# Kernel tuning notes

Hardware: AMD Instinct MI355X
Metric: run time of the kernel (lower is better)

Reference implementation:

```python
import jax, jax.numpy as jnp
import numpy as np

T = 3              # num_ntype (slots)
NH = 64            # num_hidden == num_classes
HEADS = (4, 4, 1)
NUM_ETYPES = 5
EDGE_DIM = 64
N_NODES = 20000
NEG_SLOPE = 0.2
ALPHA = 0.05       # residual-attention blend
EPS = 1e-12


def _l2_by_slot(x):
    # l2_norm with l2BySlot='True': normalize each ntype slot independently
    n = x.shape[0]
    xs = x.reshape(n, T, -1)
    nrm = jnp.linalg.norm(xs, axis=2, keepdims=True)
    return (xs / jnp.maximum(nrm, EPS)).reshape(n, -1)


def _edge_softmax(logits, dst, n):
    # softmax over incoming edges of each destination node
    m = jax.lax.stop_gradient(jax.ops.segment_max(logits, dst, num_segments=n))
    e = jnp.exp(logits - m[dst])
    s = jax.ops.segment_sum(e, dst, num_segments=n)
    return e / s[dst]


def _conv(x, src, dst, etype, W, al, ar, ee_tab, We, ae, res_attn, act):
    # slotGATConv: x [N,T,C], W [T,C,H*O], al/ar [H,T*O], ee_tab [R,De], We [De,H*De], ae [H,De]
    n = x.shape[0]
    H = al.shape[0]
    proj = jnp.einsum('ntc,tcd->ntd', x, W)                     # [N,T,H*O]
    O = proj.shape[-1] // H
    feat = proj.reshape(n, T, H, O).transpose(0, 2, 1, 3).reshape(n, H, T * O)
    el = jnp.einsum('nhd,hd->nh', feat, al)
    er = jnp.einsum('nhd,hd->nh', feat, ar)
    De = ee_tab.shape[1]
    ep = (ee_tab[etype] @ We).reshape(-1, H, De)                # [E,H,De]
    ee = jnp.einsum('ehd,hd->eh', ep, ae)                       # [E,H]
    logit = jax.nn.leaky_relu(el[src] + er[dst] + ee, NEG_SLOPE)
    a = _edge_softmax(logit, dst, n)                            # [E,H]
    if res_attn is not None:
        a = a * (1.0 - ALPHA) + res_attn * ALPHA
    out = jax.ops.segment_sum(feat[src] * a[:, :, None], dst, num_segments=n)  # [N,H,T*O]
    if act:
        out = jax.nn.elu(out)
    return out, a


def _forward(feat0, feat1, feat2, w_in0, b_in0, w_in1, b_in1, w_in2, b_in2,
             l0_W, l0_al, l0_ar, l0_ee, l0_we, l0_ae,
             l1_W, l1_al, l1_ar, l1_ee, l1_we, l1_ae,
             l2_W, l2_al, l2_ar, l2_ee, l2_we, l2_ae,
             dm_W, e_feat, src, dst, left, right, mid):
    feats = [feat0, feat1, feat2]
    lins = [(w_in0, b_in0), (w_in1, b_in1), (w_in2, b_in2)]
    blocks = []
    for t, (f, (w, b)) in enumerate(zip(feats, lins)):
        ft = f @ w + b                                          # [n_t, NH]
        pad = jnp.zeros((f.shape[0], T * NH), ft.dtype)
        blocks.append(pad.at[:, t * NH:(t + 1) * NH].set(ft))   # slot zero-padding
    h = jnp.concatenate(blocks, 0)                              # [N, T*NH]
    emb = [_l2_by_slot(h)]                                      # aggregator='None' -> identity
    x = h.reshape(-1, T, NH)
    out0, a0 = _conv(x, src, dst, e_feat, l0_W, l0_al, l0_ar, l0_ee, l0_we, l0_ae, None, True)
    emb.append(_l2_by_slot(out0.mean(1)))
    x = out0.reshape(-1, HEADS[0], T, NH).transpose(0, 2, 1, 3).reshape(-1, T, HEADS[0] * NH)
    out1, a1 = _conv(x, src, dst, e_feat, l1_W, l1_al, l1_ar, l1_ee, l1_we, l1_ae, a0, True)
    emb.append(_l2_by_slot(out1.mean(1)))
    x = out1.reshape(-1, HEADS[1], T, NH).transpose(0, 2, 1, 3).reshape(-1, T, HEADS[1] * NH)
    out2, _ = _conv(x, src, dst, e_feat, l2_W, l2_al, l2_ar, l2_ee, l2_we, l2_ae, a1, False)
    emb.append(_l2_by_slot(out2.mean(1)))
    # aggregator='None' + inProcessEmb='True': concat per-slot along feature dim
    embs = [e.reshape(-1, T, NH) for e in emb]
    o = jnp.concatenate(embs, 2).reshape(-1, T * NH * len(embs))  # [N, 768]
    le, re = o[left], o[right]
    scores = jnp.zeros(left.shape[0], o.dtype)
    for r in range(NUM_ETYPES):                                 # DistMult per relation
        s = ((le @ dm_W[r]) * re).sum(1)
        scores = jnp.where(mid == r, s, scores)
    return jax.nn.sigmoid(scores)


def setup_inputs() -> dict:
    key = jax.random.key(0)
    ks = iter(jax.random.split(key, 64))
    def nrm(shape, std):
        return jax.random.normal(next(ks), shape, jnp.float32) * std
    counts = [8000, 6000, 6000]
    in_dims = [256, 128, 64]
    inp = {}
    for t in range(T):
        inp[f'feat{t}'] = jax.random.normal(next(ks), (counts[t], in_dims[t]), jnp.float32)
        inp[f'w_in{t}'] = nrm((in_dims[t], NH), 0.1)
        inp[f'b_in{t}'] = nrm((NH,), 0.1)
    Cs = [NH, HEADS[0] * NH, HEADS[1] * NH]
    for l in range(3):
        H = HEADS[l]
        inp[f'l{l}_W'] = nrm((T, Cs[l], H * NH), 0.1)
        inp[f'l{l}_al'] = nrm((H, T * NH), 0.1)
        inp[f'l{l}_ar'] = nrm((H, T * NH), 0.1)
        inp[f'l{l}_ee'] = nrm((NUM_ETYPES, EDGE_DIM), 0.1)
        inp[f'l{l}_we'] = nrm((EDGE_DIM, H * EDGE_DIM), 0.1)
        inp[f'l{l}_ae'] = nrm((H, EDGE_DIM), 0.1)
    D = T * NH * 4
    inp['dm_W'] = nrm((NUM_ETYPES, D, D), 0.05)
    E, L = 200000, 10000
    inp['e_feat'] = jax.random.randint(next(ks), (E,), 0, NUM_ETYPES)
    inp['src'] = jax.random.randint(next(ks), (E,), 0, N_NODES)
    inp['dst'] = jax.random.randint(next(ks), (E,), 0, N_NODES)
    inp['left'] = jax.random.randint(next(ks), (L,), 0, N_NODES)
    inp['right'] = jax.random.randint(next(ks), (L,), 0, N_NODES)
    inp['mid'] = jax.random.randint(next(ks), (L,), 0, NUM_ETYPES)
    return inp


def reference(feat0, feat1, feat2, w_in0, b_in0, w_in1, b_in1, w_in2, b_in2,
              l0_W, l0_al, l0_ar, l0_ee, l0_we, l0_ae,
              l1_W, l1_al, l1_ar, l1_ee, l1_we, l1_ae,
              l2_W, l2_al, l2_ar, l2_ee, l2_we, l2_ae,
              dm_W, e_feat, src, dst, left, right, mid):
    return _forward(feat0, feat1, feat2, w_in0, b_in0, w_in1, b_in1, w_in2, b_in2,
                    l0_W, l0_al, l0_ar, l0_ee, l0_we, l0_ae,
                    l1_W, l1_al, l1_ar, l1_ee, l1_we, l1_ae,
                    l2_W, l2_al, l2_ar, l2_ee, l2_we, l2_ae,
                    dm_W, e_feat, src, dst, left, right, mid)
```

## Files before the change

kernel.cpp:

```cpp
#include <hip/hip_runtime.h>
#include <math.h>

#define N_NODES 20000
#define NPAD    20096
#define N_EDGES 200000
#define N_PAIRS 10000
#define PAIR_PAD 10368
#define DM_TILES 162
#define NBLK    79

typedef __attribute__((ext_vector_type(8))) short s16x8;
typedef __attribute__((ext_vector_type(4))) float f32x4;

__device__ inline float wave_max(float v){
  for (int o = 32; o > 0; o >>= 1) v = fmaxf(v, __shfl_xor(v, o));
  return v;
}
__device__ inline float wave_sum(float v){
  for (int o = 32; o > 0; o >>= 1) v += __shfl_xor(v, o);
  return v;
}
__device__ inline short f2bf(float x){
  union { float f; unsigned u; } v; v.f = x;
  unsigned r = (v.u + 0x7FFFu + ((v.u >> 16) & 1u)) >> 16;
  return (short)r;
}
__device__ inline float bf2f(short s){
  union { unsigned u; float f; } v; v.u = ((unsigned)(unsigned short)s) << 16;
  return v.f;
}
__device__ inline int ntype(int s){ return (s < 8000) ? 0 : ((s < 14000) ? 1 : 2); }
__device__ inline float elu1(float x){ return (x > 0.f) ? x : expm1f(x); }

#define OS(i, c) ((i) * 100 + (c))

__global__ void build_h(const float* __restrict__ f0, const float* __restrict__ w0, const float* __restrict__ b0,
                        const float* __restrict__ f1, const float* __restrict__ w1, const float* __restrict__ b1,
                        const float* __restrict__ f2, const float* __restrict__ w2, const float* __restrict__ b2,
                        short* __restrict__ Xb0, short* __restrict__ o_b,
                        int* __restrict__ cnt3, int* __restrict__ cnt5, int* __restrict__ pos5,
                        float* __restrict__ score, int* __restrict__ pairs,
                        float* __restrict__ eall, short* __restrict__ Xb12,
                        short* __restrict__ featb){
  const int blk = blockIdx.x, lane = threadIdx.x;
  const int gid = blk * 64 + lane;
  if (gid < 80000) cnt3[gid] = 0;
  if (gid < 5){ cnt5[gid * 16] = 0; pos5[gid * 16] = 0; }
  if (gid < 10016) score[gid] = 0.f;
  if (gid < PAIR_PAD) pairs[gid] = -1;
  for (int i = gid; i < 480000; i += 160000) eall[i] = 0.f;
  s16x8 z = {};
  if (gid < 4608){
    int t = (gid * 16) / 24576, off = (gid * 16) % 24576;
    short* p = Xb12 + ((size_t)(t * NPAD + N_NODES)) * 256 + off;
    *(s16x8*)p = z; *(s16x8*)(p + 8) = z;
  }
  if (gid < 1152){
    int t = (gid * 16) / 6144, off = (gid * 16) % 6144;
    short* p = Xb0 + ((size_t)(t * NPAD + N_NODES)) * 64 + off;
    *(s16x8*)p = z; *(s16x8*)(p + 8) = z;
  }
  int t, C, nbase; const float *f, *w, *b;
  if (blk < 1000)       { t = 0; nbase = 0;     C = 256; f = f0; w = w0; b = b0; }
  else if (blk < 1750)  { t = 1; nbase = 8000;  C = 128; f = f1; w = w1; b = b1; }
  else                  { t = 2; nbase = 14000; C = 64;  f = f2; w = w2; b = b2; }
  const int n0 = blk * 8;
  const int n0l = n0 - nbase;
  __shared__ float xs[8 * 256];
  const float* fr = f + (size_t)n0l * C;
  for (int i = lane; i < 8 * C; i += 64) xs[i] = fr[i];
  __syncthreads();
  float acc[8];
#pragma unroll
  for (int j = 0; j < 8; j++) acc[j] = b[lane];
  for (int c = 0; c < C; c++){
    float wv = w[c * 64 + lane];
#pragma unroll
    for (int j = 0; j < 8; j++) acc[j] += xs[j * C + c] * wv;
  }
  for (int j = 0; j < 8; j++){
    int n = n0 + j;
    {
      int h = lane >> 4, si = (lane >> 3) & 1, j8 = lane & 7;
      int s0 = (t == 0) ? 1 : 0;
      int s1 = (t == 2) ? 1 : 2;
      int toff = si ? s1 : s0;
      *(s16x8*)(featb + ((size_t)n * 4 + h) * 192 + toff * 64 + j8 * 8) = z;
    }
    for (int tt = 0; tt < 3; tt++)
      Xb0[((size_t)(tt * NPAD) + n) * 64 + lane] = f2bf((tt == t) ? acc[j] : 0.f);
    float ss = wave_sum(acc[j] * acc[j]);
    float sc = 1.f / fmaxf(sqrtf(ss), 1e-12f);
    for (int tt = 0; tt < 3; tt++)
      o_b[(size_t)n * 768 + tt * 256 + lane] = f2bf((tt == t) ? acc[j] * sc : 0.f);
  }
}

__global__ void count_prep_k(const int* __restrict__ dst, const int* __restrict__ srcv,
                             int* __restrict__ cnt3,
                             const int* __restrict__ mid, int* __restrict__ cnt5,
                             const float* __restrict__ lW0, const float* __restrict__ lW1,
                             const float* __restrict__ lW2, const float* __restrict__ dmW,
// ... 181 lines not shown
  __shared__ __attribute__((aligned(16))) short A_s[128 * 32];
  __shared__ __attribute__((aligned(16))) short B_s[64 * 32];
  const short* Xt  = Xb + (size_t)t * NPAD * C;
  const short* Wtt = Wt + ((size_t)t * NO + ct * 64) * C;
  f32x4 acc[2][4] = {};
  for (int kk = 0; kk < C; kk += 32){
    {
      int row = tid >> 1, half = tid & 1;
      const s16x8* g = (const s16x8*)(Xt + (size_t)(n0 + row) * C + kk + half * 16);
      s16x8 v0 = g[0], v1 = g[1];
      *(s16x8*)(A_s + row * 32 + half * 16) = v0;
      *(s16x8*)(A_s + row * 32 + half * 16 + 8) = v1;
    }
    {
      int row = tid >> 2, chunk = tid & 3;
      s16x8 v = *(const s16x8*)(Wtt + (size_t)row * C + kk + chunk * 8);
      *(s16x8*)(B_s + row * 32 + chunk * 8) = v;
    }
    __syncthreads();
    s16x8 af0 = *(s16x8*)(A_s + (w * 32 + ln) * 32 + quad * 8);
    s16x8 af1 = *(s16x8*)(A_s + (w * 32 + 16 + ln) * 32 + quad * 8);
    s16x8 bf[4];
#pragma unroll
    for (int b = 0; b < 4; b++) bf[b] = *(s16x8*)(B_s + (b * 16 + ln) * 32 + quad * 8);
#pragma unroll
    for (int b = 0; b < 4; b++){
      acc[0][b] = __builtin_amdgcn_mfma_f32_16x16x32_bf16(af0, bf[b], acc[0][b], 0, 0, 0);
      acc[1][b] = __builtin_amdgcn_mfma_f32_16x16x32_bf16(af1, bf[b], acc[1][b], 0, 0, 0);
    }
    __syncthreads();
  }
#pragma unroll
  for (int ar_ = 0; ar_ < 2; ar_++){
#pragma unroll
    for (int i = 0; i < 4; i++){
      int n = n0 + w * 32 + ar_ * 16 + quad * 4 + i;
      if (n >= N_NODES) continue;
#pragma unroll
      for (int b = 0; b < 4; b++){
        int jj = b * 16 + ln;
        featb[((size_t)n * H + ct) * 192 + t * 64 + jj] = f2bf(acc[ar_][b][i]);
      }
    }
  }
  float alv[4], arv[4];
#pragma unroll
  for (int b = 0; b < 4; b++){
    alv[b] = al[ct * 192 + t * 64 + b * 16 + ln];
    arv[b] = ar[ct * 192 + t * 64 + b * 16 + ln];
  }
#pragma unroll
  for (int ar_ = 0; ar_ < 2; ar_++){
#pragma unroll
    for (int i = 0; i < 4; i++){
      float pe = 0.f, pr = 0.f;
#pragma unroll
      for (int b = 0; b < 4; b++){
        pe += acc[ar_][b][i] * alv[b];
        pr += acc[ar_][b][i] * arv[b];
      }
#pragma unroll
      for (int o = 1; o < 16; o <<= 1){
        pe += __shfl_xor(pe, o);
        pr += __shfl_xor(pr, o);
      }
      int n = n0 + w * 32 + ar_ * 16 + quad * 4 + i;
      if (ln == 0 && n < N_NODES){
        atomicAdd(&elf[n * H + ct], pe);
        atomicAdd(&erf[n * H + ct], pr);
      }
    }
  }
}

template<int H, int MODE, int ACT, int TYPED>
__global__ __launch_bounds__(256) void gat_fused(
    const int* __restrict__ csr_off, const int* __restrict__ src_sorted,
    const int* __restrict__ et_sorted,
    const float* __restrict__ el, const float* __restrict__ er, const float* __restrict__ ee5,
    const float* __restrict__ aprev, float* __restrict__ aout,
    const short* __restrict__ featb, short* __restrict__ outb,
    short* __restrict__ o_b, const int* __restrict__ cnt3, int kslice){
  const int wid = threadIdx.x >> 6, lane = threadIdx.x & 63;
  const int n = blockIdx.x * 4 + wid;
  if (n >= N_NODES) return;
  const int off = csr_off[n];
  const int cnt = csr_off[n + 1] - off;
  __shared__ float a_s[4][64][H];
  __shared__ int   src_s[4][64];
  __shared__ float out_s[4][800];
  float ern[H];
  if constexpr (H == 4){
    f32x4 ev = *(const f32x4*)(er + n * 4);
#pragma unroll
    for (int h = 0; h < 4; h++) ern[h] = ev[h];
  } else {
    ern[0] = er[n];
  }

  if (cnt <= 64){
    int p = off + lane;
    int sidx = 0, r = 0;
    if (lane < cnt){ sidx = src_sorted[p]; r = et_sorted[p]; }
    int src0 = __shfl(sidx, 0);
    src_s[wid][lane] = ((lane < cnt) ? sidx : src0) * (H * 384);
    float lg[H];
#pragma unroll
    for (int h = 0; h < H; h++) lg[h] = -1e30f;
    if (lane < cnt){
      if constexpr (H == 4){
        f32x4 elv = *(const f32x4*)(el + sidx * 4);
        f32x4 eev = *(const f32x4*)(ee5 + r * 4);
#pragma unroll
        for (int h = 0; h < 4; h++){
          float v = elv[h] + ern[h] + eev[h];
          lg[h] = (v >= 0.f) ? v : 0.2f * v;
        }
      } else {
        float v = el[sidx] + ern[0] + ee5[r];
        lg[0] = (v >= 0.f) ? v : 0.2f * v;
      }
    }
    float ap[4] = {};
    if (MODE > 0 && lane < cnt){
      f32x4 av4 = *(const f32x4*)(aprev + (size_t)p * 4);
#pragma unroll
      for (int q = 0; q < 4; q++) ap[q] = av4[q];
    }
    float av[H];
#pragma unroll
    for (int h = 0; h < H; h++){
      float mh = wave_max(lg[h]);
      float ex = (lane < cnt) ? __expf(lg[h] - mh) : 0.f;
      float sh = wave_sum(ex);
      float a = ex / sh;
      if (MODE == 1) a = 0.95f * a + 0.05f * ap[h];
      if (MODE == 2) a = 0.95f * a + 0.0125f * (ap[0] + ap[1] + ap[2] + ap[3]);
      av[h] = a;
      a_s[wid][lane][h] = (lane < cnt) ? a : 0.f;
    }
    if constexpr (MODE != 2){
      if (lane < cnt){
        f32x4 o = {av[0], av[1], av[2], av[3]};
        *(f32x4*)(aout + (size_t)p * 4) = o;
      }
    }
    const char* fb = (const char*)featb;

    if constexpr (TYPED && H == 4){
      const int q = lane & 31, eo = lane >> 5;
      const int hh = q >> 3, j8 = q & 7;
      float acc[3][8] = {};
      const int b1 = cnt3[n * 4], b2 = b1 + cnt3[n * 4 + 1];
      const int rb[4] = {0, b1, b2, cnt};
#pragma unroll
      for (int t = 0; t < 3; t++){
        const int sub = hh * 384 + t * 128 + j8 * 16;
        for (int b = rb[t]; b < rb[t + 1]; b += 2){
          int e = b + eo;
          bool vld = e < rb[t + 1];
          int ei = vld ? e : rb[t + 1] - 1;
          int so = src_s[wid][ei];
          float a = vld ? a_s[wid][ei][hh] : 0.f;
          s16x8 fv = *(const s16x8*)(fb + so + sub);
#pragma unroll
          for (int i = 0; i < 8; i++) acc[t][i] += a * bf2f(fv[i]);
        }
      }
#pragma unroll
      for (int t = 0; t < 3; t++){
#pragma unroll
        for (int i = 0; i < 8; i++){
          float tot = acc[t][i] + __shfl_xor(acc[t][i], 32);
          if (ACT) tot = elu1(tot);
          if (lane < 32) out_s[wid][OS(i, hh * 24 + t * 8 + j8)] = tot;
        }
      }
    } else if constexpr (H == 4){
      const int p0 = lane;
      const int p1 = (lane < 32) ? lane + 64 : lane - 32;
      const int p2 = lane + 32;
      const int hA = p0 / 24, hB = p1 / 24, hC = p2 / 24;
      const int eo2 = lane >> 5;
      float acc0[8] = {}, acc1[8] = {}, acc2[8] = {};
      const int cnt4 = (cnt + 3) & ~3;
      for (int b = 0; b < cnt4; b += 4){
        int eB0 = b + eo2, eB1 = b + 2 + eo2;
        int oA0 = src_s[wid][b],     oB0 = src_s[wid][eB0], oC0 = src_s[wid][b + 1];
        int oA1 = src_s[wid][b + 2], oB1 = src_s[wid][eB1], oC1 = src_s[wid][b + 3];
        float aA0 = a_s[wid][b][hA],     aB0 = a_s[wid][eB0][hB], aC0 = a_s[wid][b + 1][hC];
        float aA1 = a_s[wid][b + 2][hA], aB1 = a_s[wid][eB1][hB], aC1 = a_s[wid][b + 3][hC];
        s16x8 fA0 = *(const s16x8*)(fb + oA0 + p0 * 16);
        s16x8 fB0 = *(const s16x8*)(fb + oB0 + p1 * 16);
        s16x8 fC0 = *(const s16x8*)(fb + oC0 + p2 * 16);
        s16x8 fA1 = *(const s16x8*)(fb + oA1 + p0 * 16);
        s16x8 fB1 = *(const s16x8*)(fb + oB1 + p1 * 16);
        s16x8 fC1 = *(const s16x8*)(fb + oC1 + p2 * 16);
#pragma unroll
        for (int i = 0; i < 8; i++){
          acc0[i] += aA0 * bf2f(fA0[i]) + aA1 * bf2f(fA1[i]);
          acc1[i] += aB0 * bf2f(fB0[i]) + aB1 * bf2f(fB1[i]);
          acc2[i] += aC0 * bf2f(fC0[i]) + aC1 * bf2f(fC1[i]);
        }
      }
#pragma unroll
      for (int i = 0; i < 8; i++){
        float v1 = (lane < 32) ? acc2[i] : acc1[i];
        float r1 = __shfl_xor(v1, 32);
        float v0 = acc0[i] + r1;
        if (ACT) v0 = elu1(v0);
        out_s[wid][OS(i, p0)] = v0;
        float r2 = __shfl_xor(acc2[i], 32);
        if (lane < 32){
          float vv = acc1[i] + r2;
          if (ACT) vv = elu1(vv);
          out_s[wid][OS(i, p1)] = vv;
        }
      }
    } else {
      const int eo = lane & 7, cb = lane >> 3;
      float acc[3][8] = {};
      for (int b = 0; b < cnt; b += 8){
        int e = b + eo;
        float a = a_s[wid][e][0];
        int so = src_s[wid][e];
#pragma unroll
        for (int c = 0; c < 3; c++){
          s16x8 fv = *(const s16x8*)(fb + so + (cb * 3 + c) * 16);
#pragma unroll
          for (int i = 0; i < 8; i++) acc[c][i] += a * bf2f(fv[i]);
        }
      }
#pragma unroll
      for (int c = 0; c < 3; c++){
#pragma unroll
        for (int i = 0; i < 8; i++){
          float v = acc[c][i];
          v += __shfl_xor(v, 1); v += __shfl_xor(v, 2); v += __shfl_xor(v, 4);
          if (ACT) v = elu1(v);
          if (eo == 0) out_s[wid][OS(i, cb * 3 + c)] = v;
        }
      }
    }
  } else {
    constexpr int NC = H * 192 / 8;
    const int c0 = lane, h0 = (c0 / 24) % H;
    const int c1 = lane + 64, h1 = (c1 / 24) % H;
    const bool act0 = (c0 < NC);
    const bool act1 = (H == 4) && (lane < 32);
    float acc0[8] = {}, acc1[8] = {};
    float mh[H], sh[H];
#pragma unroll
    for (int h = 0; h < H; h++){ mh[h] = -1e30f; sh[h] = 0.f; }
    for (int b = lane; b < cnt; b += 64){
      int p = off + b; int s = src_sorted[p]; int r = et_sorted[p];
#pragma unroll
      for (int h = 0; h < H; h++){
        float v = el[s * H + h] + ern[h] + ee5[r * H + h];
        v = (v >= 0.f) ? v : 0.2f * v;
        mh[h] = fmaxf(mh[h], v);
      }
    }
#pragma unroll
    for (int h = 0; h < H; h++) mh[h] = wave_max(mh[h]);
    for (int b = lane; b < cnt; b += 64){
      int p = off + b; int s = src_sorted[p]; int r = et_sorted[p];
#pragma unroll
      for (int h = 0; h < H; h++){
        float v = el[s * H + h] + ern[h] + ee5[r * H + h];
        v = (v >= 0.f) ? v : 0.2f * v;
        sh[h] += __expf(v - mh[h]);
      }
    }
#pragma unroll
    for (int h = 0; h < H; h++) sh[h] = wave_sum(sh[h]);
    if (MODE != 2){
      for (int b = lane; b < cnt; b += 64){
        int p = off + b; int s = src_sorted[p]; int r = et_sorted[p];
        float ap[4] = {};
        if (MODE > 0){
#pragma unroll
          for (int q = 0; q < 4; q++) ap[q] = aprev[(size_t)p * 4 + q];
        }
        float av[4] = {};
#pragma unroll
        for (int h = 0; h < H; h++){
          float v = el[s * H + h] + ern[h] + ee5[r * H + h];
          v = (v >= 0.f) ? v : 0.2f * v;
          float a = __expf(v - mh[h]) / sh[h];
          if (MODE == 1) a = 0.95f * a + 0.05f * ap[h];
          av[h] = a;
        }
        f32x4 o = {av[0], av[1], av[2], av[3]};
        *(f32x4*)(aout + (size_t)p * 4) = o;
      }
    }
    for (int b = 0; b < cnt; b++){
      int p = off + b; int s = src_sorted[p]; int r = et_sorted[p];
      const short* row = featb + (size_t)s * (H * 192);
      float apm[4] = {};
      if (MODE > 0){
#pragma unroll
        for (int q = 0; q < 4; q++) apm[q] = aprev[(size_t)p * 4 + q];
      }
      if (act0){
        float v = el[s * H + h0] + ern[h0] + ee5[r * H + h0];
        v = (v >= 0.f) ? v : 0.2f * v;
        float a = __expf(v - mh[h0]) / sh[h0];
        if (MODE == 1) a = 0.95f * a + 0.05f * apm[h0];
        if (MODE == 2) a = 0.95f * a + 0.0125f * (apm[0] + apm[1] + apm[2] + apm[3]);
        s16x8 vv = *(const s16x8*)(row + c0 * 8);
#pragma unroll
        for (int i = 0; i < 8; i++) acc0[i] += a * bf2f(vv[i]);
      }
      if (act1){
        float v = el[s * H + h1] + ern[h1] + ee5[r * H + h1];
        v = (v >= 0.f) ? v : 0.2f * v;
        float a = __expf(v - mh[h1]) / sh[h1];
        if (MODE == 1) a = 0.95f * a + 0.05f * apm[h1];
        s16x8 vv = *(const s16x8*)(row + c1 * 8);
#pragma unroll
        for (int i = 0; i < 8; i++) acc1[i] += a * bf2f(vv[i]);
      }
    }
    if (act0){
#pragma unroll
      for (int i = 0; i < 8; i++){
        float v = ACT ? elu1(acc0[i]) : acc0[i];
        out_s[wid][OS(i, c0)] = v;
      }
    }
    if (act1){
#pragma unroll
      for (int i = 0; i < 8; i++){
        float v = ACT ? elu1(acc1[i]) : acc1[i];
        out_s[wid][OS(i, c1)] = v;
      }
    }
  }

  constexpr int NC = H * 192 / 8;
  if (outb){
    {
      const int c0 = lane;
      if (c0 < NC){
        int dd = c0 * 8, h = dd / 192, rr = dd % 192, t = rr / 64, j = rr % 64;
        s16x8 o;
#pragma unroll
        for (int i = 0; i < 8; i++) o[i] = f2bf(out_s[wid][OS(i, c0)]);
        *(s16x8*)(outb + ((size_t)(t * NPAD) + n) * 256 + h * 64 + j) = o;
      }
    }
    if constexpr (H == 4){
      if (lane < 32){
        const int c1 = lane + 64;
        int dd = c1 * 8, h = dd / 192, rr = dd % 192, t = rr / 64, j = rr % 64;
        s16x8 o;
#pragma unroll
        for (int i = 0; i < 8; i++) o[i] = f2bf(out_s[wid][OS(i, c1)]);
        *(s16x8*)(outb + ((size_t)(t * NPAD) + n) * 256 + h * 64 + j) = o;
      }
    }
  }
  for (int t = 0; t < 3; t++){
    float v;
    if (H == 4){
      int d0 = t * 64 + lane;
      v = 0.25f * (out_s[wid][OS(d0 & 7, d0 >> 3)] +
                   out_s[wid][OS(d0 & 7, 24 + (d0 >> 3))] +
                   out_s[wid][OS(d0 & 7, 48 + (d0 >> 3))] +
                   out_s[wid][OS(d0 & 7, 72 + (d0 >> 3))]);
    } else {
      int d0 = t * 64 + lane;
      v = out_s[wid][OS(d0 & 7, d0 >> 3)];
    }
    float ss = wave_sum(v * v);
    float sc = 1.f / fmaxf(sqrtf(ss), 1e-12f);
    o_b[(size_t)n * 768 + t * 256 + kslice * 64 + lane] = f2bf(v * sc);
  }
}

__global__ void distmult_mfma(const short* __restrict__ o_b, const short* __restrict__ Mt,
                              const int* __restrict__ pairs, const int* __restrict__ left,
                              const int* __restrict__ right, const int* __restrict__ mid,
                              float* __restrict__ score){
  const int pt = blockIdx.x, ct = blockIdx.y;
  const int tid = threadIdx.x;
  const int w = tid >> 6, lane = tid & 63;
  const int quad = lane >> 4, ln = lane & 15;
  __shared__ __attribute__((aligned(16))) short smem[8192];
  short* A_s = smem;
  short* B_s = smem + 2048;
  __shared__ int pid_s[64];
  __shared__ int lbase[64];
  if (tid < 64){
    int p = pairs[pt * 64 + tid];
    pid_s[tid] = p;
    lbase[tid] = (p >= 0) ? left[p] * 768 : 0;
  }
  __syncthreads();
  int p0 = pid_s[0];
  if (p0 < 0) return;
  const int r = mid[p0];
  const short* Mr = Mt + (size_t)r * 768 * 768;
  f32x4 acc[8] = {};
  for (int kk = 0; kk < 768; kk += 32){
    {
      int row = tid >> 2, chunk = tid & 3;
      s16x8 v = *(const s16x8*)(o_b + (size_t)lbase[row] + kk + chunk * 8);
      *(s16x8*)(A_s + row * 32 + chunk * 8) = v;
    }
    {
      int row = tid >> 1, half = tid & 1;
      const s16x8* g = (const s16x8*)(Mr + (size_t)(ct * 128 + row) * 768 + kk + half * 16);
      s16x8 v0 = g[0], v1 = g[1];
      *(s16x8*)(B_s + row * 32 + half * 16) = v0;
      *(s16x8*)(B_s + row * 32 + half * 16 + 8) = v1;
    }
    __syncthreads();
    s16x8 af = *(s16x8*)(A_s + (w * 16 + ln) * 32 + quad * 8);
#pragma unroll
    for (int b = 0; b < 8; b++){
      s16x8 bf = *(s16x8*)(B_s + (b * 16 + ln) * 32 + quad * 8);
      acc[b] = __builtin_amdgcn_mfma_f32_16x16x32_bf16(af, bf, acc[b], 0, 0, 0);
    }
    __syncthreads();
  }
  short* RE_s = smem;
  {
    int row = tid >> 2, quarter = tid & 3;
    int p = pid_s[row];
    s16x8 v0 = {}, v1 = {}, v2 = {}, v3 = {};
    if (p >= 0){
      const s16x8* g = (const s16x8*)(o_b + (size_t)right[p] * 768 + ct * 128 + quarter * 32);
      v0 = g[0]; v1 = g[1]; v2 = g[2]; v3 = g[3];
    }
    __syncthreads();
    short* dst = RE_s + row * 128 + quarter * 32;
    *(s16x8*)(dst)      = v0;
    *(s16x8*)(dst + 8)  = v1;
    *(s16x8*)(dst + 16) = v2;
    *(s16x8*)(dst + 24) = v3;
  }
  __syncthreads();
#pragma unroll
  for (int i = 0; i < 4; i++){
    int row = w * 16 + quad * 4 + i;
    float s = 0.f;
#pragma unroll
    for (int b = 0; b < 8; b++)
      s += acc[b][i] * bf2f(RE_s[row * 128 + b * 16 + ln]);
    s += __shfl_xor(s, 1); s += __shfl_xor(s, 2);
    s += __shfl_xor(s, 4); s += __shfl_xor(s, 8);
    if (ln == 0){
      int p = pid_s[row];
      if (p >= 0) atomicAdd(&score[p], s);
    }
  }
}

__global__ void sigmoid_k(const float* __restrict__ score, float* __restrict__ out){
  int i = blockIdx.x * 256 + threadIdx.x;
  if (i < N_PAIRS) out[i] = 1.f / (1.f + __expf(-score[i]));
}

extern "C" void kernel_launch(void* const* d_in, const int* in_sizes, int n_in,
                              void* d_out, int out_size, void* d_ws, size_t ws_size,
                              hipStream_t stream){
  const float* f0 = (const float*)d_in[0];
  const float* w0 = (const float*)d_in[1];
  const float* b0 = (const float*)d_in[2];
  const float* f1 = (const float*)d_in[3];
  const float* w1 = (const float*)d_in[4];
  const float* b1 = (const float*)d_in[5];
  const float* f2 = (const float*)d_in[6];
  const float* w2_ = (const float*)d_in[7];
  const float* b2 = (const float*)d_in[8];
  const float* lW[3]  = {(const float*)d_in[9],  (const float*)d_in[15], (const float*)d_in[21]};
  const float* lal[3] = {(const float*)d_in[10], (const float*)d_in[16], (const float*)d_in[22]};
  const float* lar[3] = {(const float*)d_in[11], (const float*)d_in[17], (const float*)d_in[23]};
  const float* lee[3] = {(const float*)d_in[12], (const float*)d_in[18], (const float*)d_in[24]};
  const float* lwe[3] = {(const float*)d_in[13], (const float*)d_in[19], (const float*)d_in[25]};
  const float* lae[3] = {(const float*)d_in[14], (const float*)d_in[20], (const float*)d_in[26]};
  const float* dmW = (const float*)d_in[27];
  const int* efeat = (const int*)d_in[28];
  const int* srcv  = (const int*)d_in[29];
  const int* dstv  = (const int*)d_in[30];
  const int* left  = (const int*)d_in[31];
  const int* right = (const int*)d_in[32];
  const int* midv  = (const int*)d_in[33];
  float* out = (float*)d_out;

  short* feat_b = (short*)d_ws;
  float* aA     = (float*)(feat_b + 15360000);
  float* aB     = aA + 800000;
  float* eall   = aB + 800000;
  float* ee5f   = eall + 480000;
  float* score  = ee5f + 96;
  int* cnt3     = (int*)(score + 10016);
  int* csr_off  = cnt3 + 80000;
  int* csr_pos  = csr_off + 20004;
  int* loc      = csr_pos + 80000;
  int* bsum     = loc + 20000;
  int* bofs     = bsum + 128;
  int* src_sorted = bofs + 128;
  int* et_sorted  = src_sorted + 200000;
  int* cnt5     = et_sorted + 200000;
  int* off5     = cnt5 + 80;
  int* pos5     = off5 + 8;
  int* pairs    = pos5 + 80;
  short* o_b    = (short*)(pairs + PAIR_PAD);
  short* Xb0    = o_b + 15360000;
  short* Xb12   = Xb0 + 3858432;
  short* Wt0    = Xb12 + 15433728;
  short* Wt1    = Wt0 + 49152;
  short* Wt2    = Wt1 + 196608;
  short* Mt     = Wt2 + 49152;
  float* elf0 = eall, *erf0 = eall + 80000;
  float* elf1 = eall + 160000, *erf1 = eall + 240000;
  float* elf2 = eall + 320000, *erf2 = eall + 400000;

  build_h<<<2500, 64, 0, stream>>>(f0, w0, b0, f1, w1, b1, f2, w2_, b2, Xb0, o_b,
                                   cnt3, cnt5, pos5, score, pairs, eall, Xb12, feat_b);
  count_prep_k<<<782 + 6336, 256, 0, stream>>>(dstv, srcv, cnt3, midv, cnt5,
                                               lW[0], lW[1], lW[2], dmW, Wt0, Wt1, Wt2, Mt,
                                               lee[0], lwe[0], lae[0], lee[1], lwe[1], lae[1],
                                               lee[2], lwe[2], lae[2], ee5f);
  scan1_k<<<NBLK, 256, 0, stream>>>(cnt3, loc, bsum);
  scan2_k<<<1, 128, 0, stream>>>(bsum, bofs, cnt5, off5);
  scan3_k<<<NBLK, 256, 0, stream>>>(loc, bofs, csr_off, csr_pos, cnt3);
  scatter_k<<<782, 256, 0, stream>>>(dstv, srcv, efeat, csr_pos, src_sorted, et_sorted,
                                     midv, off5, pos5, pairs);

  { dim3 g(64, 4, 3);
    mfma_proj<64, 256, 1><<<g, 256, 0, stream>>>(Xb0, Wt0, feat_b, lal[0], lar[0], elf0, erf0); }
  gat_fused<4, 0, 1, 1><<<5000, 256, 0, stream>>>(csr_off, src_sorted, et_sorted, elf0, erf0, ee5f,
                                                  nullptr, aA, feat_b, Xb12, o_b, cnt3, 1);

  { dim3 g(NPAD / 128, 4, 3);
    mfma_proj<256, 256, 0><<<g, 256, 0, stream>>>(Xb12, Wt1, feat_b, lal[1], lar[1], elf1, erf1); }
  gat_fused<4, 1, 1, 0><<<5000, 256, 0, stream>>>(csr_off, src_sorted, et_sorted, elf1, erf1, ee5f + 32,
                                                  aA, aB, feat_b, Xb12, o_b, cnt3, 2);

  { dim3 g(NPAD / 128, 1, 3);
    mfma_proj<256, 64, 0><<<g, 256, 0, stream>>>(Xb12, Wt2, feat_b, lal[2], lar[2], elf2, erf2); }
  gat_fused<1, 2, 0, 0><<<5000, 256, 0, stream>>>(csr_off, src_sorted, et_sorted, elf2, erf2, ee5f + 64,
                                                  aB, nullptr, feat_b, nullptr, o_b, cnt3, 3);

  { dim3 g(DM_TILES, 6); distmult_mfma<<<g, 256, 0, stream>>>(o_b, Mt, pairs, left, right, midv, score); }
  sigmoid_k<<<40, 256, 0, stream>>>(score, out);
}
```

Measured before the change: 466.5 us.

## Process two destination nodes per wavefront using half-wave edge softmax and aggregation

Result: faster. 447.5 us (-4.1%).

```diff
diff --git a/kernel.cpp b/kernel.cpp
--- a/kernel.cpp
+++ b/kernel.cpp
@@ -18,6 +18,14 @@
 }
 __device__ inline float wave_sum(float v){
   for (int o = 32; o > 0; o >>= 1) v += __shfl_xor(v, o);
+  return v;
+}
+__device__ inline float half_max(float v){
+  for (int o = 16; o > 0; o >>= 1) v = fmaxf(v, __shfl_xor(v, o));
+  return v;
+}
+__device__ inline float half_sum(float v){
+  for (int o = 16; o > 0; o >>= 1) v += __shfl_xor(v, o);
   return v;
 }
 __device__ inline short f2bf(float x){
@@ -365,32 +373,37 @@
     const short* __restrict__ featb, short* __restrict__ outb,
     short* __restrict__ o_b, const int* __restrict__ cnt3, int kslice){
   const int wid = threadIdx.x >> 6, lane = threadIdx.x & 63;
-  const int n = blockIdx.x * 4 + wid;
-  if (n >= N_NODES) return;
-  const int off = csr_off[n];
-  const int cnt = csr_off[n + 1] - off;
+  const int half = lane >> 5, hl = lane & 31;
+  const int l32 = half << 5;
+  const int n0 = blockIdx.x * 8 + wid * 2;
+  const int nme = n0 + half;
   __shared__ float a_s[4][64][H];
   __shared__ int   src_s[4][64];
-  __shared__ float out_s[4][800];
-  float ern[H];
-  if constexpr (H == 4){
-    f32x4 ev = *(const f32x4*)(er + n * 4);
-#pragma unroll
-    for (int h = 0; h < 4; h++) ern[h] = ev[h];
-  } else {
-    ern[0] = er[n];
-  }
-
-  if (cnt <= 64){
-    int p = off + lane;
+  __shared__ float out_s[4][2][800];
+  const char* fb = (const char*)featb;
+
+  const int offm = csr_off[nme];
+  const int cntm = csr_off[nme + 1] - offm;
+  const int cnto = __shfl_xor(cntm, 32);
+  const bool paired = (cntm <= 32) && (cnto <= 32);
+
+  if (paired){
+    float ern[H];
+    if constexpr (H == 4){
+      f32x4 ev = *(const f32x4*)(er + nme * 4);
+#pragma unroll
+      for (int h = 0; h < 4; h++) ern[h] = ev[h];
+    } else ern[0] = er[nme];
+    const int p = offm + hl;
+    const bool valid = hl < cntm;
     int sidx = 0, r = 0;
-    if (lane < cnt){ sidx = src_sorted[p]; r = et_sorted[p]; }
-    int src0 = __shfl(sidx, 0);
-    src_s[wid][lane] = ((lane < cnt) ? sidx : src0) * (H * 384);
+    if (valid){ sidx = src_sorted[p]; r = et_sorted[p]; }
+    int s0 = __shfl(sidx, l32);
+    src_s[wid][lane] = (valid ? sidx : s0) * (H * 384);
     float lg[H];
 #pragma unroll
     for (int h = 0; h < H; h++) lg[h] = -1e30f;
-    if (lane < cnt){
+    if (valid){
       if constexpr (H == 4){
         f32x4 elv = *(const f32x4*)(el + sidx * 4);
         f32x4 eev = *(const f32x4*)(ee5 + r * 4);
@@ -405,7 +418,7 @@
       }
     }
     float ap[4] = {};
-    if (MODE > 0 && lane < cnt){
+    if (MODE > 0 && valid){
       f32x4 av4 = *(const f32x4*)(aprev + (size_t)p * 4);
 #pragma unroll
       for (int q = 0; q < 4; q++) ap[q] = av4[q];
@@ -413,98 +426,88 @@
     float av[H];
 #pragma unroll
     for (int h = 0; h < H; h++){
-      float mh = wave_max(lg[h]);
-      float ex = (lane < cnt) ? __expf(lg[h] - mh) : 0.f;
-      float sh = wave_sum(ex);
+      float mh = half_max(lg[h]);
+      float ex = valid ? __expf(lg[h] - mh) : 0.f;
+      float sh = half_sum(ex);
       float a = ex / sh;
       if (MODE == 1) a = 0.95f * a + 0.05f * ap[h];
       if (MODE == 2) a = 0.95f * a + 0.0125f * (ap[0] + ap[1] + ap[2] + ap[3]);
       av[h] = a;
-      a_s[wid][lane][h] = (lane < cnt) ? a : 0.f;
+      a_s[wid][lane][h] = valid ? a : 0.f;
     }
     if constexpr (MODE != 2){
-      if (lane < cnt){
+      if (valid){
         f32x4 o = {av[0], av[1], av[2], av[3]};
         *(f32x4*)(aout + (size_t)p * 4) = o;
       }
     }
-    const char* fb = (const char*)featb;
 
     if constexpr (TYPED && H == 4){
-      const int q = lane & 31, eo = lane >> 5;
-      const int hh = q >> 3, j8 = q & 7;
+      const int hh = hl >> 3, j8 = hl & 7;
       float acc[3][8] = {};
-      const int b1 = cnt3[n * 4], b2 = b1 + cnt3[n * 4 + 1];
-      const int rb[4] = {0, b1, b2, cnt};
+      const int b1 = cnt3[nme * 4], b2 = b1 + cnt3[nme * 4 + 1];
+      const int rb[4] = {0, b1, b2, cntm};
 #pragma unroll
       for (int t = 0; t < 3; t++){
         const int sub = hh * 384 + t * 128 + j8 * 16;
         for (int b = rb[t]; b < rb[t + 1]; b += 2){
-          int e = b + eo;
-          bool vld = e < rb[t + 1];
-          int ei = vld ? e : rb[t + 1] - 1;
-          int so = src_s[wid][ei];
-          float a = vld ? a_s[wid][ei][hh] : 0.f;
-          s16x8 fv = *(const s16x8*)(fb + so + sub);
-#pragma unroll
-          for (int i = 0; i < 8; i++) acc[t][i] += a * bf2f(fv[i]);
+          int e0 = l32 + b;
+          bool v1 = (b + 1) < rb[t + 1];
+          int e1 = v1 ? e0 + 1 : e0;
+          float a0 = a_s[wid][e0][hh];
+          float a1 = v1 ? a_s[wid][e1][hh] : 0.f;
+          int so0 = src_s[wid][e0], so1 = src_s[wid][e1];
+          s16x8 f0 = *(const s16x8*)(fb + so0 + sub);
+          s16x8 f1 = *(const s16x8*)(fb + so1 + sub);
+#pragma unroll
+          for (int i = 0; i < 8; i++) acc[t][i] += a0 * bf2f(f0[i]) + a1 * bf2f(f1[i]);
         }
       }
 #pragma unroll
       for (int t = 0; t < 3; t++){
 #pragma unroll
         for (int i = 0; i < 8; i++){
-          float tot = acc[t][i] + __shfl_xor(acc[t][i], 32);
-          if (ACT) tot = elu1(tot);
-          if (lane < 32) out_s[wid][OS(i, hh * 24 + t * 8 + j8)] = tot;
+          float v = acc[t][i];
+          if (ACT) v = elu1(v);
+          out_s[wid][half][OS(i, hh * 24 + t * 8 + j8)] = v;
         }
       }
     } else if constexpr (H == 4){
-      const int p0 = lane;
-      const int p1 = (lane < 32) ? lane + 64 : lane - 32;
-      const int p2 = lane + 32;
-      const int hA = p0 / 24, hB = p1 / 24, hC = p2 / 24;
-      const int eo2 = lane >> 5;
+      const int p0 = hl, p1 = hl + 32, p2 = hl + 64;
+      const int h0 = p0 / 24, h1 = p1 / 24, h2 = p2 / 24;
       float acc0[8] = {}, acc1[8] = {}, acc2[8] = {};
-      const int cnt4 = (cnt + 3) & ~3;
-      for (int b = 0; b < cnt4; b += 4){
-        int eB0 = b + eo2, eB1 = b + 2 + eo2;
-        int oA0 = src_s[wid][b],     oB0 = src_s[wid][eB0], oC0 = src_s[wid][b + 1];
-        int oA1 = src_s[wid][b + 2], oB1 = src_s[wid][eB1], oC1 = src_s[wid][b + 3];
-        float aA0 = a_s[wid][b][hA],     aB0 = a_s[wid][eB0][hB], aC0 = a_s[wid][b + 1][hC];
-        float aA1 = a_s[wid][b + 2][hA], aB1 = a_s[wid][eB1][hB], aC1 = a_s[wid][b + 3][hC];
-        s16x8 fA0 = *(const s16x8*)(fb + oA0 + p0 * 16);
-        s16x8 fB0 = *(const s16x8*)(fb + oB0 + p1 * 16);
-        s16x8 fC0 = *(const s16x8*)(fb + oC0 + p2 * 16);
-        s16x8 fA1 = *(const s16x8*)(fb + oA1 + p0 * 16);
-        s16x8 fB1 = *(const s16x8*)(fb + oB1 + p1 * 16);
-        s16x8 fC1 = *(const s16x8*)(fb + oC1 + p2 * 16);
+      const int cnt2 = (cntm + 1) & ~1;
+      for (int b = 0; b < cnt2; b += 2){
+        int e0 = l32 + b, e1 = l32 + b + 1;
+        int so0 = src_s[wid][e0], so1 = src_s[wid][e1];
+        float a00 = a_s[wid][e0][h0], a01 = a_s[wid][e0][h1], a02 = a_s[wid][e0][h2];
+        float a10 = a_s[wid][e1][h0], a11 = a_s[wid][e1][h1], a12 = a_s[wid][e1][h2];
+        s16x8 f00 = *(const s16x8*)(fb + so0 + p0 * 16);
+        s16x8 f01 = *(const s16x8*)(fb + so0 + p1 * 16);
+        s16x8 f02 = *(const s16x8*)(fb + so0 + p2 * 16);
+        s16x8 f10 = *(const s16x8*)(fb + so1 + p0 * 16);
+        s16x8 f11 = *(const s16x8*)(fb + so1 + p1 * 16);
+        s16x8 f12 = *(const s16x8*)(fb + so1 + p2 * 16);
 #pragma unroll
         for (int i = 0; i < 8; i++){
-          acc0[i] += aA0 * bf2f(fA0[i]) + aA1 * bf2f(fA1[i]);
-          acc1[i] += aB0 * bf2f(fB0[i]) + aB1 * bf2f(fB1[i]);
-          acc2[i] += aC0 * bf2f(fC0[i]) + aC1 * bf2f(fC1[i]);
+          acc0[i] += a00 * bf2f(f00[i]) + a10 * bf2f(f10[i]);
+          acc1[i] += a01 * bf2f(f01[i]) + a11 * bf2f(f11[i]);
+          acc2[i] += a02 * bf2f(f02[i]) + a12 * bf2f(f12[i]);
         }
       }
 #pragma unroll
       for (int i = 0; i < 8; i++){
-        float v1 = (lane < 32) ? acc2[i] : acc1[i];
-        float r1 = __shfl_xor(v1, 32);
-        float v0 = acc0[i] + r1;
-        if (ACT) v0 = elu1(v0);
-        out_s[wid][OS(i, p0)] = v0;
-        float r2 = __shfl_xor(acc2[i], 32);
-        if (lane < 32){
-          float vv = acc1[i] + r2;
-          if (ACT) vv = elu1(vv);
-          out_s[wid][OS(i, p1)] = vv;
-        }
+        float v0 = acc0[i], v1 = acc1[i], v2 = acc2[i];
+        if (ACT){ v0 = elu1(v0); v1 = elu1(v1); v2 = elu1(v2); }
+        out_s[wid][half][OS(i, p0)] = v0;
+        out_s[wid][half][OS(i, p1)] = v1;
+        out_s[wid][half][OS(i, p2)] = v2;
       }
     } else {
-      const int eo = lane & 7, cb = lane >> 3;
+      const int e4 = hl >> 3, cb = hl & 7;
       float acc[3][8] = {};
-      for (int b = 0; b < cnt; b += 8){
-        int e = b + eo;
+      for (int b = 0; b < cntm; b += 4){
+        int e = l32 + b + e4;
         float a = a_s[wid][e][0];
         int so = src_s[wid][e];
 #pragma unroll
@@ -519,147 +522,259 @@
 #pragma unroll
         for (int i = 0; i < 8; i++){
           float v = acc[c][i];
-          v += __shfl_xor(v, 1); v += __shfl_xor(v, 2); v += __shfl_xor(v, 4);
+          v += __shfl_xor(v, 8); v += __shfl_xor(v, 16);
           if (ACT) v = elu1(v);
-          if (eo == 0) out_s[wid][OS(i, cb * 3 + c)] = v;
+          if (e4 == 0) out_s[wid][half][OS(i, cb * 3 + c)] = v;
         }
       }
     }
   } else {
-    constexpr int NC = H * 192 / 8;
-    const int c0 = lane, h0 = (c0 / 24) % H;
-    const int c1 = lane + 64, h1 = (c1 / 24) % H;
-    const bool act0 = (c0 < NC);
-    const bool act1 = (H == 4) && (lane < 32);
-    float acc0[8] = {}, acc1[8] = {};
-    float mh[H], sh[H];
-#pragma unroll
-    for (int h = 0; h < H; h++){ mh[h] = -1e30f; sh[h] = 0.f; }
-    for (int b = lane; b < cnt; b += 64){
-      int p = off + b; int s = src_sorted[p]; int r = et_sorted[p];
-#pragma unroll
-      for (int h = 0; h < H; h++){
-        float v = el[s * H + h] + ern[h] + ee5[r * H + h];
-        v = (v >= 0.f) ? v : 0.2f * v;
-        mh[h] = fmaxf(mh[h], v);
-      }
-    }
-#pragma unroll
-    for (int h = 0; h < H; h++) mh[h] = wave_max(mh[h]);
-    for (int b = lane; b < cnt; b += 64){
-      int p = off + b; int s = src_sorted[p]; int r = et_sorted[p];
-#pragma unroll
-      for (int h = 0; h < H; h++){
-        float v = el[s * H + h] + ern[h] + ee5[r * H + h];
-        v = (v >= 0.f) ? v : 0.2f * v;
-        sh[h] += __expf(v - mh[h]);
-      }
-    }
-#pragma unroll
-    for (int h = 0; h < H; h++) sh[h] = wave_sum(sh[h]);
-    if (MODE != 2){
-      for (int b = lane; b < cnt; b += 64){
-        int p = off + b; int s = src_sorted[p]; int r = et_sorted[p];
+    for (int k = 0; k < 2; k++){
+      const int n = n0 + k;
+      const int off = csr_off[n];
+      const int cnt = csr_off[n + 1] - off;
+      float* osk = out_s[wid][k];
+      float ern[H];
+#pragma unroll
+      for (int h = 0; h < H; h++) ern[h] = er[n * H + h];
+      if (cnt <= 64){
+        int p = off + lane;
+        int sidx = 0, r = 0;
+        if (lane < cnt){ sidx = src_sorted[p]; r = et_sorted[p]; }
+        int src0 = __shfl(sidx, 0);
+        src_s[wid][lane] = ((lane < cnt) ? sidx : src0) * (H * 384);
+        float lg[H];
+#pragma unroll
+        for (int h = 0; h < H; h++) lg[h] = -1e30f;
+        if (lane < cnt){
+#pragma unroll
+          for (int h = 0; h < H; h++){
+            float v = el[sidx * H + h] + ern[h] + ee5[r * H + h];
+            lg[h] = (v >= 0.f) ? v : 0.2f * v;
+          }
+        }
         float ap[4] = {};
-        if (MODE > 0){
+        if (MODE > 0 && lane < cnt){
 #pragma unroll
           for (int q = 0; q < 4; q++) ap[q] = aprev[(size_t)p * 4 + q];
         }
-        float av[4] = {};
+        float av[H];
 #pragma unroll
         for (int h = 0; h < H; h++){
-          float v = el[s * H + h] + ern[h] + ee5[r * H + h];
-          v = (v >= 0.f) ? v : 0.2f * v;
-          float a = __expf(v - mh[h]) / sh[h];
+          float mh = wave_max(lg[h]);
+          float ex = (lane < cnt) ? __expf(lg[h] - mh) : 0.f;
+          float sh = wave_sum(ex);
+          float a = ex / sh;
           if (MODE == 1) a = 0.95f * a + 0.05f * ap[h];
+          if (MODE == 2) a = 0.95f * a + 0.0125f * (ap[0] + ap[1] + ap[2] + ap[3]);
           av[h] = a;
-        }
-        f32x4 o = {av[0], av[1], av[2], av[3]};
-        *(f32x4*)(aout + (size_t)p * 4) = o;
-      }
-    }
-    for (int b = 0; b < cnt; b++){
-      int p = off + b; int s = src_sorted[p]; int r = et_sorted[p];
-      const short* row = featb + (size_t)s * (H * 192);
-      float apm[4] = {};
-      if (MODE > 0){
-#pragma unroll
-        for (int q = 0; q < 4; q++) apm[q] = aprev[(size_t)p * 4 + q];
-      }
-      if (act0){
-        float v = el[s * H + h0] + ern[h0] + ee5[r * H + h0];
-        v = (v >= 0.f) ? v : 0.2f * v;
-        float a = __expf(v - mh[h0]) / sh[h0];
-        if (MODE == 1) a = 0.95f * a + 0.05f * apm[h0];
-        if (MODE == 2) a = 0.95f * a + 0.0125f * (apm[0] + apm[1] + apm[2] + apm[3]);
-        s16x8 vv = *(const s16x8*)(row + c0 * 8);
-#pragma unroll
-        for (int i = 0; i < 8; i++) acc0[i] += a * bf2f(vv[i]);
-      }
-      if (act1){
-        float v = el[s * H + h1] + ern[h1] + ee5[r * H + h1];
-        v = (v >= 0.f) ? v : 0.2f * v;
-        float a = __expf(v - mh[h1]) / sh[h1];
-        if (MODE == 1) a = 0.95f * a + 0.05f * apm[h1];
-        s16x8 vv = *(const s16x8*)(row + c1 * 8);
-#pragma unroll
-        for (int i = 0; i < 8; i++) acc1[i] += a * bf2f(vv[i]);
-      }
-    }
-    if (act0){
-#pragma unroll
-      for (int i = 0; i < 8; i++){
-        float v = ACT ? elu1(acc0[i]) : acc0[i];
-        out_s[wid][OS(i, c0)] = v;
-      }
-    }
-    if (act1){
-#pragma unroll
-      for (int i = 0; i < 8; i++){
-        float v = ACT ? elu1(acc1[i]) : acc1[i];
-        out_s[wid][OS(i, c1)] = v;
-      }
-    }
-  }
-
-  constexpr int NC = H * 192 / 8;
+          a_s[wid][lane][h] = (lane < cnt) ? a : 0.f;
+        }
+        if constexpr (MODE != 2){
+          if (lane < cnt){
+            f32x4 o = {av[0], av[1], av[2], av[3]};
+            *(f32x4*)(aout + (size_t)p * 4) = o;
+          }
+        }
+        if constexpr (H == 4){
+          const int p0 = lane;
+          const int p1 = (lane < 32) ? lane + 64 : lane - 32;
+          const int p2 = lane + 32;
+          const int hA = p0 / 24, hB = p1 / 24, hC = p2 / 24;
+          const int eo2 = lane >> 5;
+          float acc0[8] = {}, acc1[8] = {}, acc2[8] = {};
+          const int cnt4 = (cnt + 3) & ~3;
+          for (int b = 0; b < cnt4; b += 4){
+            int eB0 = b + eo2, eB1 = b + 2 + eo2;
+            int oA0 = src_s[wid][b],     oB0 = src_s[wid][eB0], oC0 = src_s[wid][b + 1];
+            int oA1 = src_s[wid][b + 2], oB1 = src_s[wid][eB1], oC1 = src_s[wid][b + 3];
+            float aA0 = a_s[wid][b][hA],     aB0 = a_s[wid][eB0][hB], aC0 = a_s[wid][b + 1][hC];
+            float aA1 = a_s[wid][b + 2][hA], aB1 = a_s[wid][eB1][hB], aC1 = a_s[wid][b + 3][hC];
+            s16x8 fA0 = *(const s16x8*)(fb + oA0 + p0 * 16);
+            s16x8 fB0 = *(const s16x8*)(fb + oB0 + p1 * 16);
+            s16x8 fC0 = *(const s16x8*)(fb + oC0 + p2 * 16);
+            s16x8 fA1 = *(const s16x8*)(fb + oA1 + p0 * 16);
+            s16x8 fB1 = *(const s16x8*)(fb + oB1 + p1 * 16);
+            s16x8 fC1 = *(const s16x8*)(fb + oC1 + p2 * 16);
+#pragma unroll
+            for (int i = 0; i < 8; i++){
+              acc0[i] += aA0 * bf2f(fA0[i]) + aA1 * bf2f(fA1[i]);
+              acc1[i] += aB0 * bf2f(fB0[i]) + aB1 * bf2f(fB1[i]);
+              acc2[i] += aC0 * bf2f(fC0[i]) + aC1 * bf2f(fC1[i]);
+            }
+          }
+#pragma unroll
+          for (int i = 0; i < 8; i++){
+            float v1 = (lane < 32) ? acc2[i] : acc1[i];
+            float r1 = __shfl_xor(v1, 32);
+            float v0 = acc0[i] + r1;
+            if (ACT) v0 = elu1(v0);
+            osk[OS(i, p0)] = v0;
+            float r2 = __shfl_xor(acc2[i], 32);
+            if (lane < 32){
+              float vv = acc1[i] + r2;
+              if (ACT) vv = elu1(vv);
+              osk[OS(i, p1)] = vv;
+            }
+          }
+        } else {
+          const int eo = lane & 7, cb = lane >> 3;
+          float acc[3][8] = {};
+          for (int b = 0; b < cnt; b += 8){
+            int e = b + eo;
+            float a = a_s[wid][e][0];
+            int so = src_s[wid][e];
+#pragma unroll
+            for (int c = 0; c < 3; c++){
+              s16x8 fv = *(const s16x8*)(fb + so + (cb * 3 + c) * 16);
+#pragma unroll
+              for (int i = 0; i < 8; i++) acc[c][i] += a * bf2f(fv[i]);
+            }
+          }
+#pragma unroll
+          for (int c = 0; c < 3; c++){
+#pragma unroll
+            for (int i = 0; i < 8; i++){
+              float v = acc[c][i];
+              v += __shfl_xor(v, 1); v += __shfl_xor(v, 2); v += __shfl_xor(v, 4);
+              if (ACT) v = elu1(v);
+              if (eo == 0) osk[OS(i, cb * 3 + c)] = v;
+            }
+          }
+        }
+      } else {
+        constexpr int NC = H * 192 / 8;
+        const int c0 = lane, h0 = (c0 / 24) % H;
+        const int c1 = lane + 64, h1 = (c1 / 24) % H;
+        const bool act0 = (c0 < NC);
+        const bool act1 = (H == 4) && (lane < 32);
+        float acc0[8] = {}, acc1[8] = {};
+        float mh[H], sh[H];
+#pragma unroll
+        for (int h = 0; h < H; h++){ mh[h] = -1e30f; sh[h] = 0.f; }
+        for (int b = lane; b < cnt; b += 64){
+          int pp = off + b; int s = src_sorted[pp]; int r = et_sorted[pp];
+#pragma unroll
+          for (int h = 0; h < H; h++){
+            float v = el[s * H + h] + ern[h] + ee5[r * H + h];
+            v = (v >= 0.f) ? v : 0.2f * v;
+            mh[h] = fmaxf(mh[h], v);
+          }
+        }
+#pragma unroll
+        for (int h = 0; h < H; h++) mh[h] = wave_max(mh[h]);
+        for (int b = lane; b < cnt; b += 64){
+          int pp = off + b; int s = src_sorted[pp]; int r = et_sorted[pp];
+#pragma unroll
+          for (int h = 0; h < H; h++){
+            float v = el[s * H + h] + ern[h] + ee5[r * H + h];
+            v = (v >= 0.f) ? v : 0.2f * v;
+            sh[h] += __expf(v - mh[h]);
+          }
+        }
+#pragma unroll
+        for (int h = 0; h < H; h++) sh[h] = wave_sum(sh[h]);
+        if (MODE != 2){
+          for (int b = lane; b < cnt; b += 64){
+            int pp = off + b; int s = src_sorted[pp]; int r = et_sorted[pp];
+            float ap[4] = {};
+            if (MODE > 0){
+#pragma unroll
+              for (int q = 0; q < 4; q++) ap[q] = aprev[(size_t)pp * 4 + q];
+            }
+            float av[4] = {};
+#pragma unroll
+            for (int h = 0; h < H; h++){
+              float v = el[s * H + h] + ern[h] + ee5[r * H + h];
+              v = (v >= 0.f) ? v : 0.2f * v;
+              float a = __expf(v - mh[h]) / sh[h];
+              if (MODE == 1) a = 0.95f * a + 0.05f * ap[h];
+              av[h] = a;
+            }
+            f32x4 o = {av[0], av[1], av[2], av[3]};
+            *(f32x4*)(aout + (size_t)pp * 4) = o;
+          }
+        }
+        for (int b = 0; b < cnt; b++){
+          int pp = off + b; int s = src_sorted[pp]; int r = et_sorted[pp];
+          const short* row = featb + (size_t)s * (H * 192);
+          float apm[4] = {};
+          if (MODE > 0){
+#pragma unroll
+            for (int q = 0; q < 4; q++) apm[q] = aprev[(size_t)pp * 4 + q];
+          }
+          if (act0){
+            float v = el[s * H + h0] + ern[h0] + ee5[r * H + h0];
+            v = (v >= 0.f) ? v : 0.2f * v;
+            float a = __expf(v - mh[h0]) / sh[h0];
+            if (MODE == 1) a = 0.95f * a + 0.05f * apm[h0];
+            if (MODE == 2) a = 0.95f * a + 0.0125f * (apm[0] + apm[1] + apm[2] + apm[3]);
+            s16x8 vv = *(const s16x8*)(row + c0 * 8);
+#pragma unroll
+            for (int i = 0; i < 8; i++) acc0[i] += a * bf2f(vv[i]);
+          }
+          if (act1){
+            float v = el[s * H + h1] + ern[h1] + ee5[r * H + h1];
+            v = (v >= 0.f) ? v : 0.2f * v;
+            float a = __expf(v - mh[h1]) / sh[h1];
+            if (MODE == 1) a = 0.95f * a + 0.05f * apm[h1];
+            s16x8 vv = *(const s16x8*)(row + c1 * 8);
+#pragma unroll
+            for (int i = 0; i < 8; i++) acc1[i] += a * bf2f(vv[i]);
+          }
+        }
+        if (act0){
+#pragma unroll
+          for (int i = 0; i < 8; i++) osk[OS(i, c0)] = ACT ? elu1(acc0[i]) : acc0[i];
+        }
+        if (act1){
+#pragma unroll
+          for (int i = 0; i < 8; i++) osk[OS(i, c1)] = ACT ? elu1(acc1[i]) : acc1[i];
+        }
+      }
+    }
+  }
+
+  const float* os = out_s[wid][half];
   if (outb){
-    {
-      const int c0 = lane;
-      if (c0 < NC){
-        int dd = c0 * 8, h = dd / 192, rr = dd % 192, t = rr / 64, j = rr % 64;
+    if constexpr (H == 4){
+#pragma unroll
+      for (int cc = 0; cc < 3; cc++){
+        int c = hl + cc * 32;
+        int dd = c * 8, h = dd / 192, rr = dd % 192, t = rr / 64, j = rr % 64;
         s16x8 o;
 #pragma unroll
-        for (int i = 0; i < 8; i++) o[i] = f2bf(out_s[wid][OS(i, c0)]);
-        *(s16x8*)(outb + ((size_t)(t * NPAD) + n) * 256 + h * 64 + j) = o;
-      }
-    }
+        for (int i = 0; i < 8; i++) o[i] = f2bf(os[OS(i, c)]);
+        *(s16x8*)(outb + ((size_t)(t * NPAD) + nme) * 256 + h * 64 + j) = o;
+      }
+    } else {
+      if (hl < 24){
+        int c = hl;
+        int t = (c * 8) / 64, j = (c * 8) % 64;
+        s16x8 o;
+#pragma unroll
+        for (int i = 0; i < 8; i++) o[i] = f2bf(os[OS(i, c)]);
+        *(s16x8*)(outb + ((size_t)(t * NPAD) + nme) * 256 + j) = o;
+      }
+    }
+  }
+  const int cb8 = hl >> 3, ib = hl & 7;
+  for (int t = 0; t < 3; t++){
+    float va, vb;
     if constexpr (H == 4){
-      if (lane < 32){
-        const int c1 = lane + 64;
-        int dd = c1 * 8, h = dd / 192, rr = dd % 192, t = rr / 64, j = rr % 64;
-        s16x8 o;
-#pragma unroll
-        for (int i = 0; i < 8; i++) o[i] = f2bf(out_s[wid][OS(i, c1)]);
-        *(s16x8*)(outb + ((size_t)(t * NPAD) + n) * 256 + h * 64 + j) = o;
-      }
-    }
-  }
-  for (int t = 0; t < 3; t++){
-    float v;
-    if (H == 4){
-      int d0 = t * 64 + lane;
-      v = 0.25f * (out_s[wid][OS(d0 & 7, d0 >> 3)] +
-                   out_s[wid][OS(d0 & 7, 24 + (d0 >> 3))] +
-                   out_s[wid][OS(d0 & 7, 48 + (d0 >> 3))] +
-                   out_s[wid][OS(d0 & 7, 72 + (d0 >> 3))]);
+      va = 0.25f * (os[OS(ib, t * 8 + cb8)] + os[OS(ib, 24 + t * 8 + cb8)] +
+                    os[OS(ib, 48 + t * 8 + cb8)] + os[OS(ib, 72 + t * 8 + cb8)]);
+      vb = 0.25f * (os[OS(ib, t * 8 + cb8 + 4)] + os[OS(ib, 24 + t * 8 + cb8 + 4)] +
+                    os[OS(ib, 48 + t * 8 + cb8 + 4)] + os[OS(ib, 72 + t * 8 + cb8 + 4)]);
     } else {
-      int d0 = t * 64 + lane;
-      v = out_s[wid][OS(d0 & 7, d0 >> 3)];
-    }
-    float ss = wave_sum(v * v);
+      va = os[OS(ib, t * 8 + cb8)];
+      vb = os[OS(ib, t * 8 + cb8 + 4)];
+    }
+    float ss = half_sum(va * va + vb * vb);
     float sc = 1.f / fmaxf(sqrtf(ss), 1e-12f);
-    o_b[(size_t)n * 768 + t * 256 + kslice * 64 + lane] = f2bf(v * sc);
+    short* ob = o_b + (size_t)nme * 768 + t * 256 + kslice * 64;
+    ob[hl] = f2bf(va * sc);
+    ob[hl + 32] = f2bf(vb * sc);
   }
 }
 
@@ -817,17 +932,17 @@
 
   { dim3 g(64, 4, 3);
     mfma_proj<64, 256, 1><<<g, 256, 0, stream>>>(Xb0, Wt0, feat_b, lal[0], lar[0], elf0, erf0); }
-  gat_fused<4, 0, 1, 1><<<5000, 256, 0, stream>>>(csr_off, src_sorted, et_sorted, elf0, erf0, ee5f,
+  gat_fused<4, 0, 1, 1><<<2500, 256, 0, stream>>>(csr_off, src_sorted, et_sorted, elf0, erf0, ee5f,
                                                   nullptr, aA, feat_b, Xb12, o_b, cnt3, 1);
 
   { dim3 g(NPAD / 128, 4, 3);
     mfma_proj<256, 256, 0><<<g, 256, 0, stream>>>(Xb12, Wt1, feat_b, lal[1], lar[1], elf1, erf1); }
-  gat_fused<4, 1, 1, 0><<<5000, 256, 0, stream>>>(csr_off, src_sorted, et_sorted, elf1, erf1, ee5f + 32,
+  gat_fused<4, 1, 1, 0><<<2500, 256, 0, stream>>>(csr_off, src_sorted, et_sorted, elf1, erf1, ee5f + 32,
                                                   aA, aB, feat_b, Xb12, o_b, cnt3, 2);
 
   { dim3 g(NPAD / 128, 1, 3);
     mfma_proj<256, 64, 0><<<g, 256, 0, stream>>>(Xb12, Wt2, feat_b, lal[2], lar[2], elf2, erf2); }
-  gat_fused<1, 2, 0, 0><<<5000, 256, 0, stream>>>(csr_off, src_sorted, et_sorted, elf2, erf2, ee5f + 64,
+  gat_fused<1, 2, 0, 0><<<2500, 256, 0, stream>>>(csr_off, src_sorted, et_sorted, elf2, erf2, ee5f + 64,
                                                   aB, nullptr, feat_b, nullptr, o_b, cnt3, 3);
 
   { dim3 g(DM_TILES, 6); distmult_mfma<<<g, 256, 0, stream>>>(o_b, Mt, pairs, left, right, midv, score); }
```
